# Performance work log

Hardware: AMD Instinct MI355X
Metric: run time of the kernel (lower is better)

## Reference

```python
import jax, jax.numpy as jnp
import numpy as np

WS = 4      # window_size (RSUT5 default)
SHIFT = 2   # window_size // 2
NH = 8      # num_heads
DIM = 256
H0 = W0 = T0 = 32
B0 = 1


def _ln(x, g, b, eps=1e-5):
    m = x.mean(-1, keepdims=True)
    v = ((x - m) ** 2).mean(-1, keepdims=True)
    return (x - m) / jnp.sqrt(v + eps) * g + b


def _rel_index(ws):
    c = np.stack(np.meshgrid(np.arange(ws), np.arange(ws), np.arange(ws), indexing='ij')).reshape(3, -1)
    r = (c[:, :, None] - c[:, None, :]).transpose(1, 2, 0) + (ws - 1)
    return jnp.asarray((r[..., 0] * (2 * ws - 1) + r[..., 1]) * (2 * ws - 1) + r[..., 2])


def _partition(x, ws):
    B, H, W, T, C = x.shape
    x = x.reshape(B, H // ws, ws, W // ws, ws, T // ws, ws, C)
    return x.transpose(0, 1, 3, 5, 2, 4, 6, 7).reshape(-1, ws ** 3, C)


def _reverse(w, ws, B, H, W, T):
    C = w.shape[-1]
    x = w.reshape(B, H // ws, W // ws, T // ws, ws, ws, ws, C)
    return x.transpose(0, 1, 4, 2, 5, 3, 6, 7).reshape(B, H, W, T, C)


def _attn_mask(H, W, T, ws, ss):
    # static (numpy) replica of Block.createmask; H,W,T divisible by ws here
    img = np.zeros((H, W, T), np.float32)
    sls = (slice(0, -ws), slice(-ws, -ss), slice(-ss, None))
    cnt = 0
    for h in sls:
        for w in sls:
            for t in sls:
                img[h, w, t] = cnt
                cnt += 1
    mw = img.reshape(H // ws, ws, W // ws, ws, T // ws, ws).transpose(0, 2, 4, 1, 3, 5).reshape(-1, ws ** 3)
    d = mw[:, None, :] - mw[:, :, None]
    return jnp.asarray(np.where(d != 0, -100.0, 0.0).astype(np.float32))


def _swin(x, H, W, T, shift, mask, n1g, n1b, qkvw, qkvb, rpb, projw, projb, n2g, n2b, fc1w, fc1b, fc2w, fc2b):
    B, L, C = x.shape
    N = WS ** 3
    hd = C // NH
    shortcut = x
    x = _ln(x, n1g, n1b).reshape(B, H, W, T, C)
    if shift:
        x = jnp.roll(x, (-shift, -shift, -shift), axis=(1, 2, 3))
    xw = _partition(x, WS)                                        # [B*nW, N, C]
    qkv = (xw @ qkvw.T + qkvb).reshape(-1, N, 3, NH, hd).transpose(2, 0, 3, 1, 4)
    q, k, v = qkv[0], qkv[1], qkv[2]                              # [B*nW, NH, N, hd]
    attn = jnp.einsum('bhnd,bhmd->bhnm', q * (hd ** -0.5), k)
    attn = attn + rpb[_rel_index(WS)].transpose(2, 0, 1)[None]    # relative position bias
    if mask is not None:
        nW = mask.shape[0]
        attn = (attn.reshape(B, nW, NH, N, N) + mask[None, :, None]).reshape(-1, NH, N, N)
    attn = jax.nn.softmax(attn, axis=-1)
    out = jnp.einsum('bhnm,bhmd->bhnd', attn, v).transpose(0, 2, 1, 3).reshape(-1, N, C)
    out = out @ projw.T + projb
    x = _reverse(out, WS, B, H, W, T)
    if shift:
        x = jnp.roll(x, (shift, shift, shift), axis=(1, 2, 3))
    x = shortcut + x.reshape(B, L, C)
    h = _ln(x, n2g, n2b)
    h = jax.nn.gelu(h @ fc1w.T + fc1b, approximate=False) @ fc2w.T + fc2b
    return x + h


def setup_inputs() -> dict:
    key = jax.random.key(0)
    ks = iter(jax.random.split(key, 16))
    def rn(shape, s=0.02):
        return jax.random.normal(next(ks), shape, jnp.float32) * s
    d = {'x': jax.random.normal(next(ks), (B0, H0 * W0 * T0, DIM), jnp.float32),
         'H': H0, 'W': W0, 'T': T0,
         'norm_g': jnp.ones((DIM,), jnp.float32), 'norm_b': jnp.zeros((DIM,), jnp.float32)}
    for p in ('w', 's'):
        d[p + 'n1g'] = jnp.ones((DIM,), jnp.float32); d[p + 'n1b'] = jnp.zeros((DIM,), jnp.float32)
        d[p + 'qkvw'] = rn((3 * DIM, DIM)); d[p + 'qkvb'] = jnp.zeros((3 * DIM,), jnp.float32)
        d[p + 'rpb'] = rn(((2 * WS - 1) ** 3, NH))
        d[p + 'projw'] = rn((DIM, DIM)); d[p + 'projb'] = jnp.zeros((DIM,), jnp.float32)
        d[p + 'n2g'] = jnp.ones((DIM,), jnp.float32); d[p + 'n2b'] = jnp.zeros((DIM,), jnp.float32)
        d[p + 'fc1w'] = rn((4 * DIM, DIM)); d[p + 'fc1b'] = jnp.zeros((4 * DIM,), jnp.float32)
        d[p + 'fc2w'] = rn((DIM, 4 * DIM)); d[p + 'fc2b'] = jnp.zeros((DIM,), jnp.float32)
    return d


def reference(x, H, W, T, norm_g, norm_b,
              wn1g, wn1b, wqkvw, wqkvb, wrpb, wprojw, wprojb, wn2g, wn2b, wfc1w, wfc1b, wfc2w, wfc2b,
              sn1g, sn1b, sqkvw, sqkvb, srpb, sprojw, sprojb, sn2g, sn2b, sfc1w, sfc1b, sfc2w, sfc2b):
    mask = _attn_mask(H, W, T, WS, SHIFT)
    x = _swin(x, H, W, T, 0, None, wn1g, wn1b, wqkvw, wqkvb, wrpb, wprojw, wprojb, wn2g, wn2b, wfc1w, wfc1b, wfc2w, wfc2b)
    x = _swin(x, H, W, T, SHIFT, mask, sn1g, sn1b, sqkvw, sqkvb, srpb, sprojw, sprojb, sn2g, sn2b, sfc1w, sfc1b, sfc2w, sfc2b)
    B, L, C = x.shape
    # Block.norm + toConv: [B, L, C] -> [B, C, H, W, T]
    return _ln(x, norm_g, norm_b).reshape(B, H, W, T, C).transpose(0, 4, 1, 2, 3)
```

## Files before the change

kernel.cpp:

```cpp
#include <hip/hip_runtime.h>

typedef unsigned short u16;
typedef unsigned int   u32;
typedef __bf16 bfx8 __attribute__((ext_vector_type(8)));
typedef float  fx4  __attribute__((ext_vector_type(4)));

__device__ __forceinline__ u16 f2b(float f) {
    union { float f; u32 i; } v; v.f = f;
    u32 r = (v.i + 0x7fffu + ((v.i >> 16) & 1u)) >> 16;
    return (u16)r;
}
__device__ __forceinline__ u32 pk(float a, float b) {
    return (u32)f2b(a) | ((u32)f2b(b) << 16);
}

__device__ __forceinline__ void gl2lds16(const u16* g, u16* l) {
    __builtin_amdgcn_global_load_lds(
        (const __attribute__((address_space(1))) u32*)(const void*)g,
        (__attribute__((address_space(3))) u32*)(void*)l, 16, 0, 0);
}

__device__ __forceinline__ int map_token(int r, int shift) {
    int win = r >> 6, n = r & 63;
    int wh = win >> 6, ww = (win >> 3) & 7, wt = win & 7;
    int h = wh * 4 + (n >> 4);
    int w = ww * 4 + ((n >> 2) & 3);
    int t = wt * 4 + (n & 3);
    h = (h + shift) & 31; w = (w + shift) & 31; t = (t + shift) & 31;
    return (h << 10) | (w << 5) | t;
}

struct CvtArgs { const float* src[8]; int cum[9]; };
__global__ __launch_bounds__(256) void cvt_kernel(CvtArgs a, u16* __restrict__ dst) {
    int g = (blockIdx.x * 256 + threadIdx.x) * 4;
    int t = 0;
    #pragma unroll
    for (int i = 1; i < 8; i++) t += (g >= a.cum[i]);
    int local = g - a.cum[t];
    float4 f = *(const float4*)(a.src[t] + local);
    uint2 o; o.x = pk(f.x, f.y); o.y = pk(f.z, f.w);
    *(uint2*)(dst + g) = o;
}

template<int GATHER, int F32OUT>
__global__ __launch_bounds__(256) void ln_kernel(const float* __restrict__ resid,
                                                 const float* __restrict__ g, const float* __restrict__ b,
                                                 void* __restrict__ outp, int shift) {
    int lane = threadIdx.x & 63;
    int row  = blockIdx.x * 4 + (threadIdx.x >> 6);
    int src  = GATHER ? map_token(row, shift) : row;
    float4 x = ((const float4*)(resid + src * 256))[lane];
    float s1 = x.x + x.y + x.z + x.w;
    float s2 = x.x * x.x + x.y * x.y + x.z * x.z + x.w * x.w;
    #pragma unroll
    for (int off = 1; off < 64; off <<= 1) { s1 += __shfl_xor(s1, off); s2 += __shfl_xor(s2, off); }
    float mean = s1 * (1.0f / 256.0f);
    float var  = s2 * (1.0f / 256.0f) - mean * mean;
    float rstd = rsqrtf(var + 1e-5f);
    int c = lane * 4;
    float4 gv = *(const float4*)(g + c);
    float4 bv = *(const float4*)(b + c);
    float y0 = (x.x - mean) * rstd * gv.x + bv.x;
    float y1 = (x.y - mean) * rstd * gv.y + bv.y;
    float y2 = (x.z - mean) * rstd * gv.z + bv.z;
    float y3 = (x.w - mean) * rstd * gv.w + bv.w;
    if (F32OUT) {
        float4 o; o.x = y0; o.y = y1; o.z = y2; o.w = y3;
        *(float4*)((float*)outp + row * 256 + c) = o;
    } else {
        uint2 o; o.x = pk(y0, y1); o.y = pk(y2, y3);
        *(uint2*)((u16*)outp + row * 256 + c) = o;
    }
}

template<int EPI>
__global__ __launch_bounds__(256) void gemm2(const u16* __restrict__ A, const u16* __restrict__ W,
                                             const float* __restrict__ bias,
                                             u16* __restrict__ outb, float* __restrict__ resid,
                                             int Nout, int K, int shift) {
    __shared__ u16 As[128 * 32];
    __shared__ u16 Bs[128 * 32];
    int lane = threadIdx.x & 63, w = threadIdx.x >> 6;
    int wm = w >> 1, wn = w & 1;
    int m0 = blockIdx.x * 128, n0 = blockIdx.y * 128;
    int lr = lane & 15, q = lane >> 4;
    int sw = q ^ ((lr >> 1) & 3);

    fx4 acc[4][4] = {};

    for (int kt = 0; kt < K; kt += 32) {
        __syncthreads();
        #pragma unroll
        for (int p = 0; p < 2; p++) {
            int row = p * 64 + w * 16 + (lane >> 2);
            int kg  = (lane & 3) ^ ((row >> 1) & 3);
            int slot = (p * 256 + w * 64 + lane) * 8;
            gl2lds16(A + (size_t)(m0 + row) * K + kt + kg * 8, As + slot);
            gl2lds16(W + (size_t)(n0 + row) * K + kt + kg * 8, Bs + slot);
        }
        __syncthreads();
        bfx8 af[4], bfr[4];
        #pragma unroll
        for (int t = 0; t < 4; t++) {
            int ra = wm * 64 + t * 16 + lr;
            int rb = wn * 64 + t * 16 + lr;
            af[t]  = *(const bfx8*)(As + (ra * 4 + sw) * 8);
            bfr[t] = *(const bfx8*)(Bs + (rb * 4 + sw) * 8);
        }
        #pragma unroll
        for (int i = 0; i < 4; i++)
            #pragma unroll
            for (int j = 0; j < 4; j++)
                acc[i][j] = __builtin_amdgcn_mfma_f32_16x16x32_bf16(af[i], bfr[j], acc[i][j], 0, 0, 0);
    }

    float bv[4];
    #pragma unroll
    for (int j = 0; j < 4; j++) bv[j] = bias[n0 + wn * 64 + j * 16 + lr];
    #pragma unroll
    for (int i = 0; i < 4; i++) {
        #pragma unroll
        for (int r = 0; r < 4; r++) {
            int gr = m0 + wm * 64 + i * 16 + q * 4 + r;
            int orow = (EPI == 3) ? map_token(gr, shift) : gr;
            #pragma unroll
            for (int j = 0; j < 4; j++) {
                int gc = n0 + wn * 64 + j * 16 + lr;
                float v = acc[i][j][r] + bv[j];
                if (EPI == 0) {
                    outb[(size_t)gr * Nout + gc] = f2b(v);
                } else if (EPI == 1) {
                    float gl = 0.5f * v * (1.0f + erff(v * 0.7071067811865476f));
                    outb[(size_t)gr * Nout + gc] = f2b(gl);
                } else {
                    resid[orow * 256 + gc] += v;
                }
            }
        }
    }
}

__global__ __launch_bounds__(128) void attn_mfma(const u16* __restrict__ qkv, const float* __restrict__ rpb,
                                                 u16* __restrict__ outb, int masked) {
    __shared__ u16  Pl[2][64][72];
    __shared__ u16  VT[2][32][72];
    __shared__ float rbS[2][344];
    int w = threadIdx.x >> 6;
    int lane = threadIdx.x & 63;
    int id = blockIdx.x * 2 + w;
    int win = id >> 3, head = id & 7;
    int lr = lane & 15, q = lane >> 4;

    const u16* base = qkv + (size_t)win * 64 * 768 + head * 32;

    bfx8 qf[4], kf[4];
    #pragma unroll
    for (int t = 0; t < 4; t++) {
        const u16* rq = base + (lr + 16 * t) * 768 + q * 8;
        qf[t] = *(const bfx8*)(rq);
        kf[t] = *(const bfx8*)(rq + 256);
    }
    {
        const u16* rv = base + lane * 768 + 512;
        #pragma unroll
        for (int c = 0; c < 32; c += 8) {
            bfx8 vv = *(const bfx8*)(rv + c);
            #pragma unroll
            for (int j = 0; j < 8; j++) VT[w][c + j][lane] = ((const u16*)&vv)[j];
        }
    }
    for (int i = lane; i < 343; i += 64) rbS[w][i] = rpb[i * 8 + head];

    fx4 sT[4][4] = {};
    #pragma unroll
    for (int jt = 0; jt < 4; jt++)
        #pragma unroll
        for (int it = 0; it < 4; it++)
            sT[jt][it] = __builtin_amdgcn_mfma_f32_16x16x32_bf16(kf[jt], qf[it], sT[jt][it], 0, 0, 0);

    int wh = win >> 6, ww = (win >> 3) & 7, wt = win & 7;
    const float scale = 0.17677669529663687f;

    #pragma unroll
    for (int it = 0; it < 4; it++) {
        int i = lr + 16 * it;
        int ih = i >> 4, iw = (i >> 2) & 3, iT = i & 3;
        int labn = 0;
        if (masked) {
            int lh = (wh == 7) ? (1 + (ih >> 1)) : 0;
            int lw = (ww == 7) ? (1 + (iw >> 1)) : 0;
            int lt = (wt == 7) ? (1 + (iT >> 1)) : 0;
            labn = lh * 9 + lw * 3 + lt;
        }
        float sv[4][4];
        float mx = -1e30f;
        #pragma unroll
        for (int jt = 0; jt < 4; jt++)
            #pragma unroll
            for (int r = 0; r < 4; r++) {
                int j = q * 4 + r + 16 * jt;
                int jh = j >> 4, jw = (j >> 2) & 3, jT = j & 3;
                float s = sT[jt][it][r] * scale +
                          rbS[w][((ih - jh + 3) * 7 + (iw - jw + 3)) * 7 + (iT - jT + 3)];
                if (masked) {
                    int lh = (wh == 7) ? (1 + (jh >> 1)) : 0;
                    int lw = (ww == 7) ? (1 + (jw >> 1)) : 0;
                    int lt = (wt == 7) ? (1 + (jT >> 1)) : 0;
                    if (lh * 9 + lw * 3 + lt != labn) s -= 100.0f;
                }
                sv[jt][r] = s;
                mx = fmaxf(mx, s);
            }
        mx = fmaxf(mx, __shfl_xor(mx, 16));
        mx = fmaxf(mx, __shfl_xor(mx, 32));
        float sum = 0.f;
        #pragma unroll
        for (int jt = 0; jt < 4; jt++)
            #pragma unroll
            for (int r = 0; r < 4; r++) { sv[jt][r] = __expf(sv[jt][r] - mx); sum += sv[jt][r]; }
        sum += __shfl_xor(sum, 16);
        sum += __shfl_xor(sum, 32);
        float inv = 1.0f / sum;
        #pragma unroll
        for (int jt = 0; jt < 4; jt++) {
            uint2 pw;
            pw.x = pk(sv[jt][0] * inv, sv[jt][1] * inv);
            pw.y = pk(sv[jt][2] * inv, sv[jt][3] * inv);
            *(uint2*)&Pl[w][i][q * 4 + 16 * jt] = pw;
        }
    }

    fx4 o[4][2] = {};
    #pragma unroll
    for (int kk = 0; kk < 2; kk++) {
        bfx8 pf[4], vf[2];
        #pragma unroll
        for (int it = 0; it < 4; it++) pf[it] = *(const bfx8*)&Pl[w][lr + 16 * it][q * 8 + 32 * kk];
        #pragma unroll
        for (int dt = 0; dt < 2; dt++) vf[dt] = *(const bfx8*)&VT[w][lr + 16 * dt][q * 8 + 32 * kk];
        #pragma unroll
        for (int it = 0; it < 4; it++)
            #pragma unroll
            for (int dt = 0; dt < 2; dt++)
                o[it][dt] = __builtin_amdgcn_mfma_f32_16x16x32_bf16(pf[it], vf[dt], o[it][dt], 0, 0, 0);
    }

    u16* ob = outb + (size_t)win * 64 * 256 + head * 32;
    #pragma unroll
    for (int it = 0; it < 4; it++)
        #pragma unroll
        for (int r = 0; r < 4; r++) {
            int i = 16 * it + q * 4 + r;
            #pragma unroll
            for (int dt = 0; dt < 2; dt++)
                ob[i * 256 + 16 * dt + lr] = f2b(o[it][dt][r]);
        }
}

__global__ __launch_bounds__(256) void transpose_f32(const float* __restrict__ in, float* __restrict__ out) {
    __shared__ float tile[64][65];
    int t0 = blockIdx.x * 64;
    int c0 = blockIdx.y * 64;
    int row = threadIdx.x >> 2, cg = (threadIdx.x & 3) * 16;
    const float* src = in + (t0 + row) * 256 + c0 + cg;
    #pragma unroll
    for (int j = 0; j < 16; j += 4) {
        float4 v = *(const float4*)(src + j);
        tile[row][cg + j] = v.x; tile[row][cg + j + 1] = v.y;
        tile[row][cg + j + 2] = v.z; tile[row][cg + j + 3] = v.w;
    }
    __syncthreads();
    float tmp[16];
    #pragma unroll
    for (int j = 0; j < 16; j++) tmp[j] = tile[cg + j][row];
    float* dst = out + (c0 + row) * 32768 + t0 + cg;
    #pragma unroll
    for (int j = 0; j < 4; j++) *(float4*)(dst + 4 * j) = *(float4*)(tmp + 4 * j);
}

extern "C" void kernel_launch(void* const* d_in, const int* in_sizes, int n_in,
                              void* d_out, int out_size, void* d_ws, size_t ws_size,
                              hipStream_t stream) {
    const float* x      = (const float*)d_in[0];
    const float* norm_g = (const float*)d_in[4];
    const float* norm_b = (const float*)d_in[5];

    char* wsb = (char*)d_ws;
    float* resid = (float*)wsb;
    u16*   xn    = (u16*)(wsb + (size_t)32 * 1024 * 1024);
    u16*   big   = (u16*)(wsb + (size_t)48 * 1024 * 1024);
    u16*   attnb = (u16*)(wsb + (size_t)96 * 1024 * 1024);
    u16*   wb    = (u16*)(wsb + (size_t)112 * 1024 * 1024);
    float* xnf   = (float*)(wsb + (size_t)48 * 1024 * 1024);

    CvtArgs ca;
    static const int offs[9] = {0, 196608, 262144, 524288, 786432, 983040, 1048576, 1310720, 1572864};
    for (int i = 0; i < 9; i++) ca.cum[i] = offs[i];
    ca.src[0] = (const float*)d_in[6 + 2];
    ca.src[1] = (const float*)d_in[6 + 5];
    ca.src[2] = (const float*)d_in[6 + 9];
    ca.src[3] = (const float*)d_in[6 + 11];
    ca.src[4] = (const float*)d_in[19 + 2];
    ca.src[5] = (const float*)d_in[19 + 5];
    ca.src[6] = (const float*)d_in[19 + 9];
    ca.src[7] = (const float*)d_in[19 + 11];
    cvt_kernel<<<1536, 256, 0, stream>>>(ca, wb);

    hipMemcpyAsync(resid, x, (size_t)32768 * 256 * 4, hipMemcpyDeviceToDevice, stream);

    for (int blk = 0; blk < 2; blk++) {
        void* const* P = d_in + 6 + blk * 13;
        const float* n1g  = (const float*)P[0];
        const float* n1b  = (const float*)P[1];
        const float* qkvb = (const float*)P[3];
        const float* rpb  = (const float*)P[4];
        const float* pjb  = (const float*)P[6];
        const float* n2g  = (const float*)P[7];
        const float* n2b  = (const float*)P[8];
        const float* f1b  = (const float*)P[10];
        const float* f2b_ = (const float*)P[12];
        const u16* qkvw = wb + offs[0] + blk * 786432;
        const u16* pjw  = wb + offs[1] + blk * 786432;
        const u16* f1w  = wb + offs[2] + blk * 786432;
        const u16* f2w  = wb + offs[3] + blk * 786432;
        int shift = blk ? 2 : 0;

        ln_kernel<1, 0><<<8192, 256, 0, stream>>>(resid, n1g, n1b, xn, shift);
        gemm2<0><<<dim3(256, 6), 256, 0, stream>>>(xn, qkvw, qkvb, big, nullptr, 768, 256, 0);
        attn_mfma<<<2048, 128, 0, stream>>>(big, rpb, attnb, blk);
        gemm2<3><<<dim3(256, 2), 256, 0, stream>>>(attnb, pjw, pjb, nullptr, resid, 256, 256, shift);
        ln_kernel<0, 0><<<8192, 256, 0, stream>>>(resid, n2g, n2b, xn, 0);
        gemm2<1><<<dim3(256, 8), 256, 0, stream>>>(xn, f1w, f1b, big, nullptr, 1024, 256, 0);
        gemm2<2><<<dim3(256, 2), 256, 0, stream>>>(big, f2w, f2b_, nullptr, resid, 256, 1024, 0);
    }

    ln_kernel<0, 1><<<8192, 256, 0, stream>>>(resid, norm_g, norm_b, xnf, 0);
    transpose_f32<<<dim3(512, 4), 256, 0, stream>>>(xnf, (float*)d_out);
}
```

Baseline: 513.4 us.

## Deepen GEMM K-tile, vectorize epilogues, precompute attention bias/mask tables, tanh GELU

The GEMM now loads 64-wide K tiles with an 8-way XOR swizzle and swaps the MFMA operands, so each lane holds four consecutive output columns. That lets the epilogues use packed bf16 and float4 stores and read-modify-writes. A new kernel precomputes combined relative-position-bias and shift-mask tables per head and boundary class, replacing per-element index and mask arithmetic in attention with float4 table loads. The GELU switches from erf to the tanh approximation, which changes numerics slightly. Attention output stores are also vectorized.

```diff
diff --git a/kernel.cpp b/kernel.cpp
--- a/kernel.cpp
+++ b/kernel.cpp
@@ -12,6 +12,12 @@
 }
 __device__ __forceinline__ u32 pk(float a, float b) {
     return (u32)f2b(a) | ((u32)f2b(b) << 16);
+}
+__device__ __forceinline__ float gelu(float x) {
+    float u = 0.7978845608028654f * x * (1.0f + 0.044715f * x * x);
+    float e = __expf(2.0f * u);
+    float t = 1.0f - 2.0f / (e + 1.0f);
+    return 0.5f * x * (1.0f + t);
 }
 
 __device__ __forceinline__ void gl2lds16(const u16* g, u16* l) {
@@ -40,6 +46,28 @@
     float4 f = *(const float4*)(a.src[t] + local);
     uint2 o; o.x = pk(f.x, f.y); o.y = pk(f.z, f.w);
     *(uint2*)(dst + g) = o;
+}
+
+__global__ __launch_bounds__(64) void bias_kernel(const float* __restrict__ rpbW, const float* __restrict__ rpbS,
+                                                  float* __restrict__ tab) {
+    int bx = blockIdx.x;
+    int shifted = bx >= 8;
+    int idx = shifted ? bx - 8 : bx;
+    int cls = shifted ? (idx >> 3) : 0;
+    int head = idx & 7;
+    const float* rpb = shifted ? rpbS : rpbW;
+    float* out = tab + (size_t)bx * 4096;
+    int i = threadIdx.x;
+    int ih = i >> 4, iw = (i >> 2) & 3, it = i & 3;
+    int mh = (cls >> 2) & 1, mw = (cls >> 1) & 1, mt = cls & 1;
+    int labn = (mh ? (1 + (ih >> 1)) : 0) * 9 + (mw ? (1 + (iw >> 1)) : 0) * 3 + (mt ? (1 + (it >> 1)) : 0);
+    for (int j = 0; j < 64; j++) {
+        int jh = j >> 4, jw = (j >> 2) & 3, jt = j & 3;
+        float v = rpb[(((ih - jh + 3) * 7 + (iw - jw + 3)) * 7 + (it - jt + 3)) * 8 + head];
+        int labm = (mh ? (1 + (jh >> 1)) : 0) * 9 + (mw ? (1 + (jw >> 1)) : 0) * 3 + (mt ? (1 + (jt >> 1)) : 0);
+        if (labm != labn) v -= 100.0f;
+        out[i * 64 + j] = v;
+    }
 }
 
 template<int GATHER, int F32OUT>
@@ -74,83 +102,87 @@
 }
 
 template<int EPI>
-__global__ __launch_bounds__(256) void gemm2(const u16* __restrict__ A, const u16* __restrict__ W,
+__global__ __launch_bounds__(256) void gemm3(const u16* __restrict__ A, const u16* __restrict__ W,
                                              const float* __restrict__ bias,
                                              u16* __restrict__ outb, float* __restrict__ resid,
                                              int Nout, int K, int shift) {
-    __shared__ u16 As[128 * 32];
-    __shared__ u16 Bs[128 * 32];
+    __shared__ u16 As[128 * 64];
+    __shared__ u16 Bs[128 * 64];
     int lane = threadIdx.x & 63, w = threadIdx.x >> 6;
     int wm = w >> 1, wn = w & 1;
     int m0 = blockIdx.x * 128, n0 = blockIdx.y * 128;
     int lr = lane & 15, q = lane >> 4;
-    int sw = q ^ ((lr >> 1) & 3);
 
     fx4 acc[4][4] = {};
 
-    for (int kt = 0; kt < K; kt += 32) {
+    for (int kt = 0; kt < K; kt += 64) {
         __syncthreads();
         #pragma unroll
-        for (int p = 0; p < 2; p++) {
-            int row = p * 64 + w * 16 + (lane >> 2);
-            int kg  = (lane & 3) ^ ((row >> 1) & 3);
-            int slot = (p * 256 + w * 64 + lane) * 8;
-            gl2lds16(A + (size_t)(m0 + row) * K + kt + kg * 8, As + slot);
-            gl2lds16(W + (size_t)(n0 + row) * K + kt + kg * 8, Bs + slot);
+        for (int s = 0; s < 4; s++) {
+            int p = (w * 4 + s) * 64 + lane;
+            int row = p >> 3;
+            int g = (lane & 7) ^ (row & 7);
+            gl2lds16(A + (size_t)(m0 + row) * K + kt + g * 8, As + p * 8);
+            gl2lds16(W + (size_t)(n0 + row) * K + kt + g * 8, Bs + p * 8);
         }
         __syncthreads();
-        bfx8 af[4], bfr[4];
-        #pragma unroll
-        for (int t = 0; t < 4; t++) {
-            int ra = wm * 64 + t * 16 + lr;
-            int rb = wn * 64 + t * 16 + lr;
-            af[t]  = *(const bfx8*)(As + (ra * 4 + sw) * 8);
-            bfr[t] = *(const bfx8*)(Bs + (rb * 4 + sw) * 8);
-        }
-        #pragma unroll
-        for (int i = 0; i < 4; i++)
-            #pragma unroll
-            for (int j = 0; j < 4; j++)
-                acc[i][j] = __builtin_amdgcn_mfma_f32_16x16x32_bf16(af[i], bfr[j], acc[i][j], 0, 0, 0);
-    }
-
-    float bv[4];
-    #pragma unroll
-    for (int j = 0; j < 4; j++) bv[j] = bias[n0 + wn * 64 + j * 16 + lr];
+        #pragma unroll
+        for (int kk = 0; kk < 2; kk++) {
+            bfx8 af[4], bfr[4];
+            #pragma unroll
+            for (int t = 0; t < 4; t++) {
+                int ra = wm * 64 + t * 16 + lr;
+                int pa = (q + 4 * kk) ^ (ra & 7);
+                af[t] = *(const bfx8*)(As + ra * 64 + pa * 8);
+                int rb2 = wn * 64 + t * 16 + lr;
+                int pb = (q + 4 * kk) ^ (rb2 & 7);
+                bfr[t] = *(const bfx8*)(Bs + rb2 * 64 + pb * 8);
+            }
+            #pragma unroll
+            for (int i = 0; i < 4; i++)
+                #pragma unroll
+                for (int j = 0; j < 4; j++)
+                    acc[i][j] = __builtin_amdgcn_mfma_f32_16x16x32_bf16(bfr[j], af[i], acc[i][j], 0, 0, 0);
+        }
+    }
+
+    float4 bv[4];
+    #pragma unroll
+    for (int j = 0; j < 4; j++) bv[j] = *(const float4*)(bias + n0 + wn * 64 + j * 16 + q * 4);
     #pragma unroll
     for (int i = 0; i < 4; i++) {
-        #pragma unroll
-        for (int r = 0; r < 4; r++) {
-            int gr = m0 + wm * 64 + i * 16 + q * 4 + r;
-            int orow = (EPI == 3) ? map_token(gr, shift) : gr;
-            #pragma unroll
-            for (int j = 0; j < 4; j++) {
-                int gc = n0 + wn * 64 + j * 16 + lr;
-                float v = acc[i][j][r] + bv[j];
-                if (EPI == 0) {
-                    outb[(size_t)gr * Nout + gc] = f2b(v);
-                } else if (EPI == 1) {
-                    float gl = 0.5f * v * (1.0f + erff(v * 0.7071067811865476f));
-                    outb[(size_t)gr * Nout + gc] = f2b(gl);
-                } else {
-                    resid[orow * 256 + gc] += v;
-                }
+        int gr = m0 + wm * 64 + i * 16 + lr;
+        int orow = (EPI == 3) ? map_token(gr, shift) : gr;
+        #pragma unroll
+        for (int j = 0; j < 4; j++) {
+            int gc = n0 + wn * 64 + j * 16 + q * 4;
+            float v0 = acc[i][j][0] + bv[j].x;
+            float v1 = acc[i][j][1] + bv[j].y;
+            float v2 = acc[i][j][2] + bv[j].z;
+            float v3 = acc[i][j][3] + bv[j].w;
+            if (EPI == 0) {
+                uint2 o; o.x = pk(v0, v1); o.y = pk(v2, v3);
+                *(uint2*)(outb + (size_t)gr * Nout + gc) = o;
+            } else if (EPI == 1) {
+                uint2 o; o.x = pk(gelu(v0), gelu(v1)); o.y = pk(gelu(v2), gelu(v3));
+                *(uint2*)(outb + (size_t)gr * Nout + gc) = o;
+            } else {
+                float4 rv = *(float4*)(resid + orow * 256 + gc);
+                rv.x += v0; rv.y += v1; rv.z += v2; rv.w += v3;
+                *(float4*)(resid + orow * 256 + gc) = rv;
             }
         }
     }
 }
 
-__global__ __launch_bounds__(128) void attn_mfma(const u16* __restrict__ qkv, const float* __restrict__ rpb,
-                                                 u16* __restrict__ outb, int masked) {
-    __shared__ u16  Pl[2][64][72];
-    __shared__ u16  VT[2][32][72];
-    __shared__ float rbS[2][344];
-    int w = threadIdx.x >> 6;
-    int lane = threadIdx.x & 63;
+__global__ __launch_bounds__(128) void attn3(const u16* __restrict__ qkv, const float* __restrict__ tab,
+                                             u16* __restrict__ outb, int masked) {
+    __shared__ u16 Pl[2][64][72];
+    __shared__ u16 VT[2][32][72];
+    int w = threadIdx.x >> 6, lane = threadIdx.x & 63;
     int id = blockIdx.x * 2 + w;
     int win = id >> 3, head = id & 7;
     int lr = lane & 15, q = lane >> 4;
-
     const u16* base = qkv + (size_t)win * 64 * 768 + head * 32;
 
     bfx8 qf[4], kf[4];
@@ -169,7 +201,6 @@
             for (int j = 0; j < 8; j++) VT[w][c + j][lane] = ((const u16*)&vv)[j];
         }
     }
-    for (int i = lane; i < 343; i += 64) rbS[w][i] = rpb[i * 8 + head];
 
     fx4 sT[4][4] = {};
     #pragma unroll
@@ -179,38 +210,26 @@
             sT[jt][it] = __builtin_amdgcn_mfma_f32_16x16x32_bf16(kf[jt], qf[it], sT[jt][it], 0, 0, 0);
 
     int wh = win >> 6, ww = (win >> 3) & 7, wt = win & 7;
+    int slab = masked ? (8 + ((((wh == 7) ? 4 : 0) | ((ww == 7) ? 2 : 0) | ((wt == 7) ? 1 : 0)) * 8) + head)
+                      : head;
+    const float* bt = tab + (size_t)slab * 4096 + q * 4;
     const float scale = 0.17677669529663687f;
 
     #pragma unroll
     for (int it = 0; it < 4; it++) {
         int i = lr + 16 * it;
-        int ih = i >> 4, iw = (i >> 2) & 3, iT = i & 3;
-        int labn = 0;
-        if (masked) {
-            int lh = (wh == 7) ? (1 + (ih >> 1)) : 0;
-            int lw = (ww == 7) ? (1 + (iw >> 1)) : 0;
-            int lt = (wt == 7) ? (1 + (iT >> 1)) : 0;
-            labn = lh * 9 + lw * 3 + lt;
-        }
+        const float* br = bt + i * 64;
         float sv[4][4];
         float mx = -1e30f;
         #pragma unroll
-        for (int jt = 0; jt < 4; jt++)
-            #pragma unroll
-            for (int r = 0; r < 4; r++) {
-                int j = q * 4 + r + 16 * jt;
-                int jh = j >> 4, jw = (j >> 2) & 3, jT = j & 3;
-                float s = sT[jt][it][r] * scale +
-                          rbS[w][((ih - jh + 3) * 7 + (iw - jw + 3)) * 7 + (iT - jT + 3)];
-                if (masked) {
-                    int lh = (wh == 7) ? (1 + (jh >> 1)) : 0;
-                    int lw = (ww == 7) ? (1 + (jw >> 1)) : 0;
-                    int lt = (wt == 7) ? (1 + (jT >> 1)) : 0;
-                    if (lh * 9 + lw * 3 + lt != labn) s -= 100.0f;
-                }
-                sv[jt][r] = s;
-                mx = fmaxf(mx, s);
-            }
+        for (int jt = 0; jt < 4; jt++) {
+            float4 bb = *(const float4*)(br + 16 * jt);
+            sv[jt][0] = sT[jt][it][0] * scale + bb.x;
+            sv[jt][1] = sT[jt][it][1] * scale + bb.y;
+            sv[jt][2] = sT[jt][it][2] * scale + bb.z;
+            sv[jt][3] = sT[jt][it][3] * scale + bb.w;
+            mx = fmaxf(mx, fmaxf(fmaxf(sv[jt][0], sv[jt][1]), fmaxf(sv[jt][2], sv[jt][3])));
+        }
         mx = fmaxf(mx, __shfl_xor(mx, 16));
         mx = fmaxf(mx, __shfl_xor(mx, 32));
         float sum = 0.f;
@@ -242,19 +261,21 @@
         for (int it = 0; it < 4; it++)
             #pragma unroll
             for (int dt = 0; dt < 2; dt++)
-                o[it][dt] = __builtin_amdgcn_mfma_f32_16x16x32_bf16(pf[it], vf[dt], o[it][dt], 0, 0, 0);
+                o[it][dt] = __builtin_amdgcn_mfma_f32_16x16x32_bf16(vf[dt], pf[it], o[it][dt], 0, 0, 0);
     }
 
     u16* ob = outb + (size_t)win * 64 * 256 + head * 32;
     #pragma unroll
-    for (int it = 0; it < 4; it++)
-        #pragma unroll
-        for (int r = 0; r < 4; r++) {
-            int i = 16 * it + q * 4 + r;
-            #pragma unroll
-            for (int dt = 0; dt < 2; dt++)
-                ob[i * 256 + 16 * dt + lr] = f2b(o[it][dt][r]);
-        }
+    for (int it = 0; it < 4; it++) {
+        int i = lr + 16 * it;
+        #pragma unroll
+        for (int dt = 0; dt < 2; dt++) {
+            uint2 ov;
+            ov.x = pk(o[it][dt][0], o[it][dt][1]);
+            ov.y = pk(o[it][dt][2], o[it][dt][3]);
+            *(uint2*)(ob + i * 256 + dt * 16 + q * 4) = ov;
+        }
+    }
 }
 
 __global__ __launch_bounds__(256) void transpose_f32(const float* __restrict__ in, float* __restrict__ out) {
@@ -291,6 +312,7 @@
     u16*   big   = (u16*)(wsb + (size_t)48 * 1024 * 1024);
     u16*   attnb = (u16*)(wsb + (size_t)96 * 1024 * 1024);
     u16*   wb    = (u16*)(wsb + (size_t)112 * 1024 * 1024);
+    float* tab   = (float*)(wsb + (size_t)115 * 1024 * 1024);
     float* xnf   = (float*)(wsb + (size_t)48 * 1024 * 1024);
 
     CvtArgs ca;
@@ -305,6 +327,7 @@
     ca.src[6] = (const float*)d_in[19 + 9];
     ca.src[7] = (const float*)d_in[19 + 11];
     cvt_kernel<<<1536, 256, 0, stream>>>(ca, wb);
+    bias_kernel<<<72, 64, 0, stream>>>((const float*)d_in[6 + 4], (const float*)d_in[19 + 4], tab);
 
     hipMemcpyAsync(resid, x, (size_t)32768 * 256 * 4, hipMemcpyDeviceToDevice, stream);
 
@@ -313,7 +336,6 @@
         const float* n1g  = (const float*)P[0];
         const float* n1b  = (const float*)P[1];
         const float* qkvb = (const float*)P[3];
-        const float* rpb  = (const float*)P[4];
         const float* pjb  = (const float*)P[6];
         const float* n2g  = (const float*)P[7];
         const float* n2b  = (const float*)P[8];
@@ -326,12 +348,12 @@
         int shift = blk ? 2 : 0;
 
         ln_kernel<1, 0><<<8192, 256, 0, stream>>>(resid, n1g, n1b, xn, shift);
-        gemm2<0><<<dim3(256, 6), 256, 0, stream>>>(xn, qkvw, qkvb, big, nullptr, 768, 256, 0);
-        attn_mfma<<<2048, 128, 0, stream>>>(big, rpb, attnb, blk);
-        gemm2<3><<<dim3(256, 2), 256, 0, stream>>>(attnb, pjw, pjb, nullptr, resid, 256, 256, shift);
+        gemm3<0><<<dim3(256, 6), 256, 0, stream>>>(xn, qkvw, qkvb, big, nullptr, 768, 256, 0);
+        attn3<<<2048, 128, 0, stream>>>(big, tab, attnb, blk);
+        gemm3<3><<<dim3(256, 2), 256, 0, stream>>>(attnb, pjw, pjb, nullptr, resid, 256, 256, shift);
         ln_kernel<0, 0><<<8192, 256, 0, stream>>>(resid, n2g, n2b, xn, 0);
-        gemm2<1><<<dim3(256, 8), 256, 0, stream>>>(xn, f1w, f1b, big, nullptr, 1024, 256, 0);
-        gemm2<2><<<dim3(256, 2), 256, 0, stream>>>(big, f2w, f2b_, nullptr, resid, 256, 1024, 0);
+        gemm3<1><<<dim3(256, 8), 256, 0, stream>>>(xn, f1w, f1b, big, nullptr, 1024, 256, 0);
+        gemm3<2><<<dim3(256, 2), 256, 0, stream>>>(big, f2w, f2b_, nullptr, resid, 256, 1024, 0);
     }
 
     ln_kernel<0, 1><<<8192, 256, 0, stream>>>(resid, norm_g, norm_b, xnf, 0);
```

Result: slower. 545.9 us (+6.3%).
